# Kernel optimization log

Measured on AMD Instinct MI355X. Metric: run time of the kernel, lower is better.

## Reference

```python
import jax, jax.numpy as jnp
from jax import lax
import numpy as np

WIN = 15
PAD = WIN // 2  # floor(15/2) = 7


def _box_sum(x):
    """Sum over a 15x15 window, stride 1, zero padding 7 (same as F.conv2d
    with an all-ones [1,1,15,15] filter). Done separably (H then W) for
    efficiency; math is identical to the dense ones-filter conv."""
    kh = jnp.ones((1, 1, WIN, 1), x.dtype)
    kw = jnp.ones((1, 1, 1, WIN), x.dtype)
    x = lax.conv_general_dilated(x, kh, (1, 1), [(PAD, PAD), (0, 0)])
    x = lax.conv_general_dilated(x, kw, (1, 1), [(0, 0), (PAD, PAD)])
    return x


def setup_inputs() -> dict:
    key = jax.random.key(0)
    k1, k2 = jax.random.split(key)
    B, C, H, W = 16, 1, 512, 512
    I = jax.random.uniform(k1, (B, C, H, W), dtype=jnp.float32)
    J = jax.random.uniform(k2, (B, C, H, W), dtype=jnp.float32)
    return {"I": I, "J": J}


def reference(I, J):
    win_size = jnp.asarray(WIN * WIN, I.dtype)

    I_sum = _box_sum(I)
    J_sum = _box_sum(J)
    I2_sum = _box_sum(I * I)
    J2_sum = _box_sum(J * J)
    IJ_sum = _box_sum(I * J)

    u_I = I_sum / win_size
    u_J = J_sum / win_size

    cross = IJ_sum - u_J * I_sum - u_I * J_sum + u_I * u_J * win_size
    I_var = I2_sum - 2 * u_I * I_sum + u_I * u_I * win_size
    J_var = J2_sum - 2 * u_J * J_sum + u_J * u_J * win_size

    # NOTE: faithful to the torch code — cc is a GLOBAL scalar ratio,
    # so torch.mean(cc) == cc.
    cc = jnp.sum(cross) / jnp.sqrt(jnp.sum(I_var) * jnp.sum(J_var))
    return -cc
```

## Files before the change

### kernel.cpp

```cpp
#include <hip/hip_runtime.h>
#include <math.h>


#define IMG_H 512
#define IMG_W 512
#define NB    16
#define TW    64
#define TH    32
#define HALO  7
#define SPAN_R 46
#define SPAN_C 80
#define LSTR  80
#define VSTR  82
#define NTX   8
#define NTY   16
#define NBLK  (NB * NTX * NTY)

__device__ __forceinline__ float winw(int i) {
    int a = i < 7 ? i : 7;
    int b = (511 - i) < 7 ? (511 - i) : 7;
    return (float)(a + b + 1);
}

__global__ __launch_bounds__(256) void ncc_main(const float* __restrict__ I,
                                                const float* __restrict__ J,
                                                float* __restrict__ partials) {
    __shared__ float lI[SPAN_R * LSTR];
    __shared__ float lJ[SPAN_R * LSTR];
    __shared__ float vI[TH * VSTR];
    __shared__ float vJ[TH * VSTR];
    __shared__ float red[4 * 6];

    const int tid = threadIdx.x;
    const int tx = blockIdx.x, ty = blockIdx.y, bz = blockIdx.z;
    const int R0 = ty * TH - HALO;
    const int C0 = tx * TW - 8;
    const float* Ib = I + (size_t)bz * IMG_H * IMG_W;
    const float* Jb = J + (size_t)bz * IMG_H * IMG_W;

    float a0 = 0.f, a1 = 0.f, a2 = 0.f;

    for (int k = tid; k < SPAN_R * (SPAN_C / 4); k += 256) {
        int r = k / (SPAN_C / 4);
        int q = k - r * (SPAN_C / 4);
        int gr = R0 + r;
        int gc4 = C0 + q * 4;
        float4 iv = make_float4(0.f, 0.f, 0.f, 0.f);
        float4 jv = make_float4(0.f, 0.f, 0.f, 0.f);
        if ((unsigned)gr < (unsigned)IMG_H && (unsigned)gc4 < (unsigned)IMG_W) {
            const float4* ip = reinterpret_cast<const float4*>(Ib + gr * IMG_W + gc4);
            const float4* jp = reinterpret_cast<const float4*>(Jb + gr * IMG_W + gc4);
            iv = *ip;
            jv = *jp;
        }
        reinterpret_cast<float4*>(lI)[r * (LSTR / 4) + q] = iv;
        reinterpret_cast<float4*>(lJ)[r * (LSTR / 4) + q] = jv;
        if (r >= HALO && r < HALO + TH && q >= 2 && q < 18) {
            float wr = winw(gr);
            float w0 = wr * winw(gc4 + 0);
            float w1 = wr * winw(gc4 + 1);
            float w2 = wr * winw(gc4 + 2);
            float w3 = wr * winw(gc4 + 3);
            a0 += iv.x * jv.x * w0 + iv.y * jv.y * w1 + iv.z * jv.z * w2 + iv.w * jv.w * w3;
            a1 += iv.x * iv.x * w0 + iv.y * iv.y * w1 + iv.z * iv.z * w2 + iv.w * iv.w * w3;
            a2 += jv.x * jv.x * w0 + jv.y * jv.y * w1 + jv.z * jv.z * w2 + jv.w * jv.w * w3;
        }
    }
    __syncthreads();

    {
        int p = tid % 40;
        int chunk = tid / 40;
        if (chunk < 6) {
            int r0 = (chunk < 4) ? chunk * 6 : 24 + (chunk - 4) * 4;
            int nr = (chunk < 4) ? 6 : 4;
            const float2* lI2 = reinterpret_cast<const float2*>(lI);
            const float2* lJ2 = reinterpret_cast<const float2*>(lJ);
            float2* vI2 = reinterpret_cast<float2*>(vI);
            float2* vJ2 = reinterpret_cast<float2*>(vJ);
            float2 sI = make_float2(0.f, 0.f), sJ = make_float2(0.f, 0.f);
            #pragma unroll
            for (int dr = 0; dr < 15; ++dr) {
                float2 i2 = lI2[(r0 + dr) * 40 + p];
                float2 j2 = lJ2[(r0 + dr) * 40 + p];
                sI.x += i2.x; sI.y += i2.y;
                sJ.x += j2.x; sJ.y += j2.y;
            }
            vI2[r0 * 41 + p] = sI;
            vJ2[r0 * 41 + p] = sJ;
            for (int r = r0 + 1; r < r0 + nr; ++r) {
                float2 iA = lI2[(r + 14) * 40 + p], iB = lI2[(r - 1) * 40 + p];
                float2 jA = lJ2[(r + 14) * 40 + p], jB = lJ2[(r - 1) * 40 + p];
                sI.x += iA.x - iB.x; sI.y += iA.y - iB.y;
                sJ.x += jA.x - jB.x; sJ.y += jA.y - jB.y;
                vI2[r * 41 + p] = sI;
                vJ2[r * 41 + p] = sJ;
            }
        }
    }
    __syncthreads();

    float a3 = 0.f, a4 = 0.f, a5 = 0.f;
    {
        int r = tid & 31;
        int ch = tid >> 5;
        int c0 = ch * 8;
        int base = r * VSTR + c0;
        const float2* vI2 = reinterpret_cast<const float2*>(vI);
        const float2* vJ2 = reinterpret_cast<const float2*>(vJ);
        float va[22], vb[22];
        va[0] = vI[base + 1];  vb[0] = vJ[base + 1];
        #pragma unroll
        for (int i = 0; i < 10; ++i) {
            float2 x = vI2[(base + 2) / 2 + i];
            float2 y = vJ2[(base + 2) / 2 + i];
            va[1 + 2 * i] = x.x; va[2 + 2 * i] = x.y;
            vb[1 + 2 * i] = y.x; vb[2 + 2 * i] = y.y;
        }
        va[21] = vI[base + 22]; vb[21] = vJ[base + 22];

        float sI = 0.0f, sJ = 0.0f;
        #pragma unroll
        for (int i = 0; i < 15; ++i) { sI += va[i]; sJ += vb[i]; }
        a3 += sI * sJ;
        a4 += sI * sI;
        a5 += sJ * sJ;
        #pragma unroll
        for (int i = 1; i < 8; ++i) {
            sI += va[i + 14] - va[i - 1];
            sJ += vb[i + 14] - vb[i - 1];
            a3 += sI * sJ;
            a4 += sI * sI;
            a5 += sJ * sJ;
        }
    }

    float vals[6] = {a0, a1, a2, a3, a4, a5};
    #pragma unroll
    for (int k = 0; k < 6; ++k) {
        float v = vals[k];
        #pragma unroll
        for (int off = 32; off > 0; off >>= 1) v += __shfl_down(v, off, 64);
        vals[k] = v;
    }
    int wave = tid >> 6, lane = tid & 63;
    if (lane == 0) {
        #pragma unroll
        for (int k = 0; k < 6; ++k) red[wave * 6 + k] = vals[k];
    }
    __syncthreads();
    if (tid == 0) {
        int bidx = (bz * NTY + ty) * NTX + tx;
        #pragma unroll
        for (int k = 0; k < 6; ++k) {
            partials[bidx * 6 + k] = red[k] + red[6 + k] + red[12 + k] + red[18 + k];
        }
    }
}

__global__ __launch_bounds__(256) void ncc_finalize(const float* __restrict__ partials,
                                                    float* __restrict__ out) {
    __shared__ double red[4 * 6];
    int tid = threadIdx.x;
    double acc[6] = {0, 0, 0, 0, 0, 0};
    for (int b = tid; b < NBLK; b += 256) {
        #pragma unroll
        for (int k = 0; k < 6; ++k) acc[k] += (double)partials[b * 6 + k];
    }
    #pragma unroll
    for (int k = 0; k < 6; ++k) {
        double v = acc[k];
        #pragma unroll
        for (int off = 32; off > 0; off >>= 1) v += __shfl_down(v, off, 64);
        acc[k] = v;
    }
    int wave = tid >> 6, lane = tid & 63;
    if (lane == 0) {
        #pragma unroll
        for (int k = 0; k < 6; ++k) red[wave * 6 + k] = acc[k];
    }
    __syncthreads();
    if (tid == 0) {
        double s[6];
        #pragma unroll
        for (int k = 0; k < 6; ++k) s[k] = red[k] + red[6 + k] + red[12 + k] + red[18 + k];
        double A = s[0], Bv = s[1], Cv = s[2], D = s[3], E = s[4], F = s[5];
        double num = A - D / 225.0;
        double varI = Bv - E / 225.0;
        double varJ = Cv - F / 225.0;
        double cc = num / sqrt(varI * varJ);
        out[0] = (float)(-cc);
    }
}

extern "C" void kernel_launch(void* const* d_in, const int* in_sizes, int n_in,
                              void* d_out, int out_size, void* d_ws, size_t ws_size,
                              hipStream_t stream) {
    const float* I = (const float*)d_in[0];
    const float* J = (const float*)d_in[1];
    float* partials = (float*)d_ws;

    dim3 grid(NTX, NTY, NB);
    ncc_main<<<grid, 256, 0, stream>>>(I, J, partials);
    ncc_finalize<<<1, 256, 0, stream>>>(partials, (float*)d_out);
}
```

Baseline: 91.74 us.

## Do horizontal box sums in registers from global loads, vertical pass from LDS

Each thread now loads a 32-wide row segment of I and J straight into registers and computes the horizontal 15-wide sliding sums there, writing only those sums to shared memory. This removes the raw-tile LDS staging buffers and one full LDS round trip. The vertical pass then reads the horizontal sums column-wise from LDS. Launch bounds now request 4 blocks per CU, and the partials use a struct-of-arrays layout so the finalize kernel can read them as float4. The trade-off is higher register pressure from the 32-element arrays and redundant halo loads across threads.

```diff
diff --git a/kernel.cpp b/kernel.cpp
--- a/kernel.cpp
+++ b/kernel.cpp
@@ -7,11 +7,8 @@
 #define NB    16
 #define TW    64
 #define TH    32
-#define HALO  7
-#define SPAN_R 46
-#define SPAN_C 80
-#define LSTR  80
-#define VSTR  82
+#define HR    46
+#define HSTR  68
 #define NTX   8
 #define NTY   16
 #define NBLK  (NB * NTX * NTY)
@@ -22,79 +19,84 @@
     return (float)(a + b + 1);
 }
 
-__global__ __launch_bounds__(256) void ncc_main(const float* __restrict__ I,
-                                                const float* __restrict__ J,
-                                                float* __restrict__ partials) {
-    __shared__ float lI[SPAN_R * LSTR];
-    __shared__ float lJ[SPAN_R * LSTR];
-    __shared__ float vI[TH * VSTR];
-    __shared__ float vJ[TH * VSTR];
+__global__ __launch_bounds__(256, 4) void ncc_main(const float* __restrict__ I,
+                                                   const float* __restrict__ J,
+                                                   float* __restrict__ partials) {
+    __shared__ float hI[HR * HSTR];
+    __shared__ float hJ[HR * HSTR];
     __shared__ float red[4 * 6];
 
     const int tid = threadIdx.x;
     const int tx = blockIdx.x, ty = blockIdx.y, bz = blockIdx.z;
-    const int R0 = ty * TH - HALO;
-    const int C0 = tx * TW - 8;
     const float* Ib = I + (size_t)bz * IMG_H * IMG_W;
     const float* Jb = J + (size_t)bz * IMG_H * IMG_W;
 
     float a0 = 0.f, a1 = 0.f, a2 = 0.f;
 
-    for (int k = tid; k < SPAN_R * (SPAN_C / 4); k += 256) {
-        int r = k / (SPAN_C / 4);
-        int q = k - r * (SPAN_C / 4);
-        int gr = R0 + r;
-        int gc4 = C0 + q * 4;
-        float4 iv = make_float4(0.f, 0.f, 0.f, 0.f);
-        float4 jv = make_float4(0.f, 0.f, 0.f, 0.f);
-        if ((unsigned)gr < (unsigned)IMG_H && (unsigned)gc4 < (unsigned)IMG_W) {
-            const float4* ip = reinterpret_cast<const float4*>(Ib + gr * IMG_W + gc4);
-            const float4* jp = reinterpret_cast<const float4*>(Jb + gr * IMG_W + gc4);
-            iv = *ip;
-            jv = *jp;
-        }
-        reinterpret_cast<float4*>(lI)[r * (LSTR / 4) + q] = iv;
-        reinterpret_cast<float4*>(lJ)[r * (LSTR / 4) + q] = jv;
-        if (r >= HALO && r < HALO + TH && q >= 2 && q < 18) {
-            float wr = winw(gr);
-            float w0 = wr * winw(gc4 + 0);
-            float w1 = wr * winw(gc4 + 1);
-            float w2 = wr * winw(gc4 + 2);
-            float w3 = wr * winw(gc4 + 3);
-            a0 += iv.x * jv.x * w0 + iv.y * jv.y * w1 + iv.z * jv.z * w2 + iv.w * jv.w * w3;
-            a1 += iv.x * iv.x * w0 + iv.y * iv.y * w1 + iv.z * iv.z * w2 + iv.w * iv.w * w3;
-            a2 += jv.x * jv.x * w0 + jv.y * jv.y * w1 + jv.z * jv.z * w2 + jv.w * jv.w * w3;
-        }
-    }
-    __syncthreads();
+    {
+        int r = tid >> 2;
+        int k = tid & 3;
+        if (r < HR) {
+            int gr = ty * TH - 7 + r;
+            int cb = tx * TW + 16 * k - 8;
+            bool rok = (unsigned)gr < (unsigned)IMG_H;
+            const float* Irow = Ib + gr * IMG_W;
+            const float* Jrow = Jb + gr * IMG_W;
 
-    {
-        int p = tid % 40;
-        int chunk = tid / 40;
-        if (chunk < 6) {
-            int r0 = (chunk < 4) ? chunk * 6 : 24 + (chunk - 4) * 4;
-            int nr = (chunk < 4) ? 6 : 4;
-            const float2* lI2 = reinterpret_cast<const float2*>(lI);
-            const float2* lJ2 = reinterpret_cast<const float2*>(lJ);
-            float2* vI2 = reinterpret_cast<float2*>(vI);
-            float2* vJ2 = reinterpret_cast<float2*>(vJ);
-            float2 sI = make_float2(0.f, 0.f), sJ = make_float2(0.f, 0.f);
+            float xI[32], xJ[32];
             #pragma unroll
-            for (int dr = 0; dr < 15; ++dr) {
-                float2 i2 = lI2[(r0 + dr) * 40 + p];
-                float2 j2 = lJ2[(r0 + dr) * 40 + p];
-                sI.x += i2.x; sI.y += i2.y;
-                sJ.x += j2.x; sJ.y += j2.y;
+            for (int i = 0; i < 8; ++i) {
+                int gc = cb + 4 * i;
+                float4 iv = make_float4(0.f, 0.f, 0.f, 0.f);
+                float4 jv = make_float4(0.f, 0.f, 0.f, 0.f);
+                if (rok && (unsigned)gc < (unsigned)IMG_W) {
+                    iv = *reinterpret_cast<const float4*>(Irow + gc);
+                    jv = *reinterpret_cast<const float4*>(Jrow + gc);
+                }
+                xI[4 * i + 0] = iv.x; xI[4 * i + 1] = iv.y;
+                xI[4 * i + 2] = iv.z; xI[4 * i + 3] = iv.w;
+                xJ[4 * i + 0] = jv.x; xJ[4 * i + 1] = jv.y;
+                xJ[4 * i + 2] = jv.z; xJ[4 * i + 3] = jv.w;
             }
-            vI2[r0 * 41 + p] = sI;
-            vJ2[r0 * 41 + p] = sJ;
-            for (int r = r0 + 1; r < r0 + nr; ++r) {
-                float2 iA = lI2[(r + 14) * 40 + p], iB = lI2[(r - 1) * 40 + p];
-                float2 jA = lJ2[(r + 14) * 40 + p], jB = lJ2[(r - 1) * 40 + p];
-                sI.x += iA.x - iB.x; sI.y += iA.y - iB.y;
-                sJ.x += jA.x - jB.x; sJ.y += jA.y - jB.y;
-                vI2[r * 41 + p] = sI;
-                vJ2[r * 41 + p] = sJ;
+
+            float sI = 0.f, sJ = 0.f;
+            #pragma unroll
+            for (int m = 1; m <= 15; ++m) { sI += xI[m]; sJ += xJ[m]; }
+
+            float* hIp = hI + r * HSTR + 16 * k;
+            float* hJp = hJ + r * HSTR + 16 * k;
+            #pragma unroll
+            for (int t = 0; t < 4; ++t) {
+                float4 bI, bJ;
+                #pragma unroll
+                for (int u = 0; u < 4; ++u) {
+                    int j = 4 * t + u;
+                    if (j > 0) {
+                        sI += xI[j + 15] - xI[j];
+                        sJ += xJ[j + 15] - xJ[j];
+                    }
+                    (&bI.x)[u] = sI;
+                    (&bJ.x)[u] = sJ;
+                }
+                *reinterpret_cast<float4*>(hIp + 4 * t) = bI;
+                *reinterpret_cast<float4*>(hJp + 4 * t) = bJ;
+            }
+
+            if (r >= 7 && r < 7 + TH) {
+                float wr = winw(gr);
+                float p0 = 0.f, p1 = 0.f, p2 = 0.f;
+                #pragma unroll
+                for (int j = 0; j < 16; ++j) {
+                    float wc = winw(tx * TW + 16 * k + j);
+                    float Iv = xI[j + 8];
+                    float Jv = xJ[j + 8];
+                    p0 += Iv * Jv * wc;
+                    p1 += Iv * Iv * wc;
+                    p2 += Jv * Jv * wc;
+                }
+                a0 += wr * p0;
+                a1 += wr * p1;
+                a2 += wr * p2;
             }
         }
     }
@@ -102,36 +104,23 @@
 
     float a3 = 0.f, a4 = 0.f, a5 = 0.f;
     {
-        int r = tid & 31;
-        int ch = tid >> 5;
-        int c0 = ch * 8;
-        int base = r * VSTR + c0;
-        const float2* vI2 = reinterpret_cast<const float2*>(vI);
-        const float2* vJ2 = reinterpret_cast<const float2*>(vJ);
-        float va[22], vb[22];
-        va[0] = vI[base + 1];  vb[0] = vJ[base + 1];
+        int col = tid & 63;
+        int chunk = tid >> 6;
+        int c8 = chunk * 8;
+        const float* pI = hI + c8 * HSTR + col;
+        const float* pJ = hJ + c8 * HSTR + col;
+        float sI = 0.f, sJ = 0.f;
         #pragma unroll
-        for (int i = 0; i < 10; ++i) {
-            float2 x = vI2[(base + 2) / 2 + i];
-            float2 y = vJ2[(base + 2) / 2 + i];
-            va[1 + 2 * i] = x.x; va[2 + 2 * i] = x.y;
-            vb[1 + 2 * i] = y.x; vb[2 + 2 * i] = y.y;
+        for (int dr = 0; dr < 15; ++dr) {
+            sI += pI[dr * HSTR];
+            sJ += pJ[dr * HSTR];
         }
-        va[21] = vI[base + 22]; vb[21] = vJ[base + 22];
-
-        float sI = 0.0f, sJ = 0.0f;
+        a3 += sI * sJ; a4 += sI * sI; a5 += sJ * sJ;
         #pragma unroll
-        for (int i = 0; i < 15; ++i) { sI += va[i]; sJ += vb[i]; }
-        a3 += sI * sJ;
-        a4 += sI * sI;
-        a5 += sJ * sJ;
-        #pragma unroll
-        for (int i = 1; i < 8; ++i) {
-            sI += va[i + 14] - va[i - 1];
-            sJ += vb[i + 14] - vb[i - 1];
-            a3 += sI * sJ;
-            a4 += sI * sI;
-            a5 += sJ * sJ;
+        for (int s = 1; s < 8; ++s) {
+            sI += pI[(14 + s) * HSTR] - pI[(s - 1) * HSTR];
+            sJ += pJ[(14 + s) * HSTR] - pJ[(s - 1) * HSTR];
+            a3 += sI * sJ; a4 += sI * sI; a5 += sJ * sJ;
         }
     }
 
@@ -153,7 +142,7 @@
         int bidx = (bz * NTY + ty) * NTX + tx;
         #pragma unroll
         for (int k = 0; k < 6; ++k) {
-            partials[bidx * 6 + k] = red[k] + red[6 + k] + red[12 + k] + red[18 + k];
+            partials[k * NBLK + bidx] = red[k] + red[6 + k] + red[12 + k] + red[18 + k];
         }
     }
 }
@@ -163,9 +152,13 @@
     __shared__ double red[4 * 6];
     int tid = threadIdx.x;
     double acc[6] = {0, 0, 0, 0, 0, 0};
-    for (int b = tid; b < NBLK; b += 256) {
-        #pragma unroll
-        for (int k = 0; k < 6; ++k) acc[k] += (double)partials[b * 6 + k];
+    #pragma unroll
+    for (int k = 0; k < 6; ++k) {
+        const float4* p = reinterpret_cast<const float4*>(partials + k * NBLK);
+        for (int t = tid; t < NBLK / 4; t += 256) {
+            float4 v = p[t];
+            acc[k] += (double)v.x + (double)v.y + (double)v.z + (double)v.w;
+        }
     }
     #pragma unroll
     for (int k = 0; k < 6; ++k) {
```

Measured after the change: 92.23 us. About the same (+0.5%).
